# Performance work log

Measured on AMD Instinct MI355X. Metric: run time of the kernel, lower is better.

## Reference

```python
import jax, jax.numpy as jnp
import numpy as np

# SMPL-style 24-joint kinematic tree (parents[j] < j, root has parent -1)
PARENTS = [-1, 0, 0, 0, 1, 2, 3, 4, 5, 6, 7, 8, 9, 9, 9, 12, 13, 14, 16, 17, 18, 19, 20, 21]
B, J = 524288, 24


def setup_inputs() -> dict:
    key = jax.random.key(0)
    k1, k2 = jax.random.split(key)
    rotations = jax.random.normal(k1, (B, J, 4), dtype=jnp.float32)
    initial_skeleton = jax.random.normal(k2, (J, 3), dtype=jnp.float32)
    return {"rotations": rotations, "initial_skeleton": initial_skeleton}


def quat_to_matrix(q):
    # q: [..., 4] (w, x, y, z) -> R: [..., 3, 3]. Faithful to the torch code
    # (no normalization of the quaternion).
    w, x, y, z = q[..., 0], q[..., 1], q[..., 2], q[..., 3]
    r00 = 1 - 2 * (y * y + z * z)
    r01 = 2 * (x * y - z * w)
    r02 = 2 * (x * z + y * w)
    r10 = 2 * (x * y + z * w)
    r11 = 1 - 2 * (x * x + z * z)
    r12 = 2 * (y * z - x * w)
    r20 = 2 * (x * z - y * w)
    r21 = 2 * (y * z + x * w)
    r22 = 1 - 2 * (x * x + y * y)
    row0 = jnp.stack([r00, r01, r02], axis=-1)
    row1 = jnp.stack([r10, r11, r12], axis=-1)
    row2 = jnp.stack([r20, r21, r22], axis=-1)
    return jnp.stack([row0, row1, row2], axis=-2)


def reference(rotations, initial_skeleton):
    # rotations: [B, J, 4] -> joints: [B, J, 3]
    parents = np.asarray(PARENTS)
    # Per-joint bone offset in rest pose; root gets skel[0]-skel[0] = 0.
    offsets = initial_skeleton - initial_skeleton[np.maximum(parents, 0)]  # [J, 3]
    R = quat_to_matrix(rotations)                                          # [B, J, 3, 3]
    # Rotate each bone offset by the joint's own rotation (as in the source),
    # fully parallel across batch and joints.
    rotated = jnp.einsum('bjik,jk->bji', R, offsets)                       # [B, J, 3]
    # Accumulate along the tree (J=24 is a small structural loop).
    b = rotations.shape[0]
    pos = [None] * len(parents)
    pos[0] = jnp.zeros((b, 3), dtype=rotations.dtype)
    for j in range(1, len(parents)):
        pos[j] = pos[parents[j]] + rotated[:, j]
    return jnp.stack(pos, axis=1)  # [B, J, 3]
```

## Files before the change

### kernel.cpp

```cpp
#include <hip/hip_runtime.h>

typedef float floatx4 __attribute__((ext_vector_type(4)));

__device__ __constant__ int cP1[24] = {0,0,0,0,1,2,3,4,5,6,7,8,9,9,9,12,13,14,16,17,18,19,20,21};
__device__ __constant__ int cP2[24] = {0,0,0,0,0,0,0,1,2,3,4,5,6,6,6,9,9,9,13,14,16,17,18,19};
__device__ __constant__ int cP4[24] = {0,0,0,0,0,0,0,0,0,0,0,0,0,0,0,3,3,3,6,6,9,9,13,14};

#define ITERS 16

__global__ __launch_bounds__(256, 8) void fk_kernel(
    const float* __restrict__ rot,
    const float* __restrict__ skel,
    float* __restrict__ out,
    int B)
{
    const int tid = threadIdx.x;
    const int j   = tid & 31;
    const int grp = tid >> 5;
    const bool act = j < 24;
    const int jc  = act ? j : 0;

    const int p1 = cP1[jc];
    const int p2 = cP2[jc];
    const int p4 = cP4[jc];

    const int sA = (4 * j) / 3;
    const int sB = (sA < 23) ? sA + 1 : 23;
    const int r  = j % 3;

    const float sx = skel[jc * 3 + 0];
    const float sy = skel[jc * 3 + 1];
    const float sz = skel[jc * 3 + 2];
    const float ox = sx - __shfl(sx, p1, 32);
    const float oy = sy - __shfl(sy, p1, 32);
    const float oz = sz - __shfl(sz, p1, 32);

    const float4* __restrict__ rot4 = reinterpret_cast<const float4*>(rot);
    floatx4* __restrict__ out4 = reinterpret_cast<floatx4*>(out);

    const int base = blockIdx.x * (8 * ITERS);

    int b = base + grp;
    float4 q = make_float4(0.f, 0.f, 0.f, 0.f);
    if (act && b < B) q = rot4[(size_t)b * 24 + j];

    for (int it = 0; it < ITERS; ++it) {
        const int bn = base + (it + 1) * 8 + grp;
        float4 qn = make_float4(0.f, 0.f, 0.f, 0.f);
        if (it + 1 < ITERS && act && bn < B) qn = rot4[(size_t)bn * 24 + j];

        if (b < B) {
            const float w = q.x, x = q.y, y = q.z, z = q.w;
            float vx = (1.f - 2.f * (y * y + z * z)) * ox
                     + (2.f * (x * y - z * w)) * oy
                     + (2.f * (x * z + y * w)) * oz;
            float vy = (2.f * (x * y + z * w)) * ox
                     + (1.f - 2.f * (x * x + z * z)) * oy
                     + (2.f * (y * z - x * w)) * oz;
            float vz = (2.f * (x * z - y * w)) * ox
                     + (2.f * (y * z + x * w)) * oy
                     + (1.f - 2.f * (x * x + y * y)) * oz;

            float ax = vx + __shfl(vx, p1, 32);
            float ay = vy + __shfl(vy, p1, 32);
            float az = vz + __shfl(vz, p1, 32);

            float bx = ax + __shfl(ax, p2, 32);
            float by = ay + __shfl(ay, p2, 32);
            float bz = az + __shfl(az, p2, 32);

            float cx = bx + __shfl(bx, p4, 32);
            float cy = by + __shfl(by, p4, 32);
            float cz = bz + __shfl(bz, p4, 32);

            const float axA = __shfl(cx, sA, 32), ayA = __shfl(cy, sA, 32), azA = __shfl(cz, sA, 32);
            const float axB = __shfl(cx, sB, 32), ayB = __shfl(cy, sB, 32), azB = __shfl(cz, sB, 32);

            const float o0 = (r == 0) ? axA : (r == 1) ? ayA : azA;
            const float o1 = (r == 0) ? ayA : (r == 1) ? azA : axB;
            const float o2 = (r == 0) ? azA : (r == 1) ? axB : ayB;
            const float o3 = (r == 0) ? axB : (r == 1) ? ayB : azB;

            if (j < 18) {
                floatx4 v; v.x = o0; v.y = o1; v.z = o2; v.w = o3;
                __builtin_nontemporal_store(v, out4 + (size_t)b * 18 + j);
            }
        }
        q = qn;
        b = bn;
    }
}

extern "C" void kernel_launch(void* const* d_in, const int* in_sizes, int n_in,
                              void* d_out, int out_size, void* d_ws, size_t ws_size,
                              hipStream_t stream) {
    const float* rot  = (const float*)d_in[0];
    const float* skel = (const float*)d_in[1];
    float* out = (float*)d_out;

    const int B = in_sizes[0] / (24 * 4);
    const int perBlock = 8 * ITERS;
    const int grid = (B + perBlock - 1) / perBlock;
    fk_kernel<<<grid, 256, 0, stream>>>(rot, skel, out, B);
}
```

Before: 58.81 us.

## Replace two shuffle-scan levels with redundant ancestor quaternion loads and rotations

Each lane now loads the quaternions of its first three ancestors and rotates their bone offsets directly, summing four rotated offsets in registers. Only one shuffle step (to the fourth ancestor) remains, replacing the three-level pointer-jumping shuffle scan. The manual register prefetch is dropped in favour of unroll-by-4 with more occupancy headroom (launch bounds 8 -> 4). This trades shuffle latency for 4x the quaternion loads (mostly cache hits within a batch row) and more ALU work in a memory-bound kernel.

```diff
diff --git a/kernel.cpp b/kernel.cpp
--- a/kernel.cpp
+++ b/kernel.cpp
@@ -2,13 +2,23 @@
 
 typedef float floatx4 __attribute__((ext_vector_type(4)));
 
-__device__ __constant__ int cP1[24] = {0,0,0,0,1,2,3,4,5,6,7,8,9,9,9,12,13,14,16,17,18,19,20,21};
-__device__ __constant__ int cP2[24] = {0,0,0,0,0,0,0,1,2,3,4,5,6,6,6,9,9,9,13,14,16,17,18,19};
-__device__ __constant__ int cP4[24] = {0,0,0,0,0,0,0,0,0,0,0,0,0,0,0,3,3,3,6,6,9,9,13,14};
+__device__ __constant__ int cA1[24] = {0,0,0,0,1,2,3,4,5,6,7,8,9,9,9,12,13,14,16,17,18,19,20,21};
+__device__ __constant__ int cA2[24] = {0,0,0,0,0,0,0,1,2,3,4,5,6,6,6,9,9,9,13,14,16,17,18,19};
+__device__ __constant__ int cA3[24] = {0,0,0,0,0,0,0,0,0,0,1,2,3,3,3,6,6,6,9,9,13,14,16,17};
+__device__ __constant__ int cA4[24] = {0,0,0,0,0,0,0,0,0,0,0,0,0,0,0,3,3,3,6,6,9,9,13,14};
 
 #define ITERS 16
 
-__global__ __launch_bounds__(256, 8) void fk_kernel(
+__device__ __forceinline__ void qrot_acc(const float4 q,
+                                         const float ox, const float oy, const float oz,
+                                         float& vx, float& vy, float& vz) {
+    const float w = q.x, x = q.y, y = q.z, z = q.w;
+    vx += (1.f - 2.f * (y * y + z * z)) * ox + (2.f * (x * y - z * w)) * oy + (2.f * (x * z + y * w)) * oz;
+    vy += (2.f * (x * y + z * w)) * ox + (1.f - 2.f * (x * x + z * z)) * oy + (2.f * (y * z - x * w)) * oz;
+    vz += (2.f * (x * z - y * w)) * ox + (2.f * (y * z + x * w)) * oy + (1.f - 2.f * (x * x + y * y)) * oz;
+}
+
+__global__ __launch_bounds__(256, 4) void fk_kernel(
     const float* __restrict__ rot,
     const float* __restrict__ skel,
     float* __restrict__ out,
@@ -17,61 +27,48 @@
     const int tid = threadIdx.x;
     const int j   = tid & 31;
     const int grp = tid >> 5;
-    const bool act = j < 24;
-    const int jc  = act ? j : 0;
+    const int jc  = (j < 24) ? j : 0;
 
-    const int p1 = cP1[jc];
-    const int p2 = cP2[jc];
-    const int p4 = cP4[jc];
+    const int a1 = cA1[jc], a2 = cA2[jc], a3 = cA3[jc], a4 = cA4[jc];
+
+    const float sJx = skel[jc * 3 + 0], sJy = skel[jc * 3 + 1], sJz = skel[jc * 3 + 2];
+    const float s1x = skel[a1 * 3 + 0], s1y = skel[a1 * 3 + 1], s1z = skel[a1 * 3 + 2];
+    const float s2x = skel[a2 * 3 + 0], s2y = skel[a2 * 3 + 1], s2z = skel[a2 * 3 + 2];
+    const float s3x = skel[a3 * 3 + 0], s3y = skel[a3 * 3 + 1], s3z = skel[a3 * 3 + 2];
+    const float s4x = skel[a4 * 3 + 0], s4y = skel[a4 * 3 + 1], s4z = skel[a4 * 3 + 2];
+    const float oSx = sJx - s1x, oSy = sJy - s1y, oSz = sJz - s1z;
+    const float o1x = s1x - s2x, o1y = s1y - s2y, o1z = s1z - s2z;
+    const float o2x = s2x - s3x, o2y = s2y - s3y, o2z = s2z - s3z;
+    const float o3x = s3x - s4x, o3y = s3y - s4y, o3z = s3z - s4z;
 
     const int sA = (4 * j) / 3;
     const int sB = (sA < 23) ? sA + 1 : 23;
     const int r  = j % 3;
-
-    const float sx = skel[jc * 3 + 0];
-    const float sy = skel[jc * 3 + 1];
-    const float sz = skel[jc * 3 + 2];
-    const float ox = sx - __shfl(sx, p1, 32);
-    const float oy = sy - __shfl(sy, p1, 32);
-    const float oz = sz - __shfl(sz, p1, 32);
 
     const float4* __restrict__ rot4 = reinterpret_cast<const float4*>(rot);
     floatx4* __restrict__ out4 = reinterpret_cast<floatx4*>(out);
 
     const int base = blockIdx.x * (8 * ITERS);
 
-    int b = base + grp;
-    float4 q = make_float4(0.f, 0.f, 0.f, 0.f);
-    if (act && b < B) q = rot4[(size_t)b * 24 + j];
+#pragma unroll 4
+    for (int it = 0; it < ITERS; ++it) {
+        const int b = base + it * 8 + grp;
+        if (b < B) {
+            const size_t b24 = (size_t)b * 24;
+            const float4 qS = rot4[b24 + jc];
+            const float4 q1 = rot4[b24 + a1];
+            const float4 q2 = rot4[b24 + a2];
+            const float4 q3 = rot4[b24 + a3];
 
-    for (int it = 0; it < ITERS; ++it) {
-        const int bn = base + (it + 1) * 8 + grp;
-        float4 qn = make_float4(0.f, 0.f, 0.f, 0.f);
-        if (it + 1 < ITERS && act && bn < B) qn = rot4[(size_t)bn * 24 + j];
+            float vx = 0.f, vy = 0.f, vz = 0.f;
+            qrot_acc(qS, oSx, oSy, oSz, vx, vy, vz);
+            qrot_acc(q1, o1x, o1y, o1z, vx, vy, vz);
+            qrot_acc(q2, o2x, o2y, o2z, vx, vy, vz);
+            qrot_acc(q3, o3x, o3y, o3z, vx, vy, vz);
 
-        if (b < B) {
-            const float w = q.x, x = q.y, y = q.z, z = q.w;
-            float vx = (1.f - 2.f * (y * y + z * z)) * ox
-                     + (2.f * (x * y - z * w)) * oy
-                     + (2.f * (x * z + y * w)) * oz;
-            float vy = (2.f * (x * y + z * w)) * ox
-                     + (1.f - 2.f * (x * x + z * z)) * oy
-                     + (2.f * (y * z - x * w)) * oz;
-            float vz = (2.f * (x * z - y * w)) * ox
-                     + (2.f * (y * z + x * w)) * oy
-                     + (1.f - 2.f * (x * x + y * y)) * oz;
-
-            float ax = vx + __shfl(vx, p1, 32);
-            float ay = vy + __shfl(vy, p1, 32);
-            float az = vz + __shfl(vz, p1, 32);
-
-            float bx = ax + __shfl(ax, p2, 32);
-            float by = ay + __shfl(ay, p2, 32);
-            float bz = az + __shfl(az, p2, 32);
-
-            float cx = bx + __shfl(bx, p4, 32);
-            float cy = by + __shfl(by, p4, 32);
-            float cz = bz + __shfl(bz, p4, 32);
+            const float cx = vx + __shfl(vx, a4, 32);
+            const float cy = vy + __shfl(vy, a4, 32);
+            const float cz = vz + __shfl(vz, a4, 32);
 
             const float axA = __shfl(cx, sA, 32), ayA = __shfl(cy, sA, 32), azA = __shfl(cz, sA, 32);
             const float axB = __shfl(cx, sB, 32), ayB = __shfl(cy, sB, 32), azB = __shfl(cz, sB, 32);
@@ -86,8 +83,6 @@
                 __builtin_nontemporal_store(v, out4 + (size_t)b * 18 + j);
             }
         }
-        q = qn;
-        b = bn;
     }
 }
 
```

After: 71.90 us. +22.3%, slower.
